# Optimization experiments

Hardware: AMD Instinct MI355X
Metric: run time of the kernel (lower is better)

## Reference

```python
import jax, jax.numpy as jnp
import numpy as np

H = 32          # num_attention_heads
D_NOPE = 128    # qk_nope_head_dim
D_ROPE = 64     # qk_rope_head_dim
D_Q = D_NOPE + D_ROPE  # 192, q_head_dim
D_V = 128       # v_head_dim
R_KV = 512      # kv_lora_rank
EPS = 1e-6


def setup_inputs() -> dict:
    key = jax.random.key(0)
    ks = jax.random.split(key, 5)
    return {
        "hidden_states": jax.random.normal(ks[0], (2, 4096, 4096), jnp.float32),
        "q_a_w": jax.random.normal(ks[1], (1536, 4096), jnp.float32) * 0.02,
        "q_b_w": jax.random.normal(ks[2], (H * D_Q, 1536), jnp.float32) * 0.02,
        "kv_a_w": jax.random.normal(ks[3], (R_KV + D_ROPE, 4096), jnp.float32) * 0.02,
        "kv_b_w": jax.random.normal(ks[4], (H * (D_NOPE + D_V), R_KV), jnp.float32) * 0.02,
        "q_a_ln_w": jnp.ones((1536,), jnp.float32),
        "kv_a_ln_w": jnp.ones((R_KV,), jnp.float32),
    }


def _rmsnorm(x, w):
    xf = x.astype(jnp.float32)
    var = jnp.mean(xf * xf, axis=-1, keepdims=True)
    return (w * (xf * jax.lax.rsqrt(var + EPS))).astype(x.dtype)


def _deepseek_transpose(x):
    # interleave swap on last dim: view (..., d//2, 2) -> transpose -> (..., d)
    b, h, s, d = x.shape
    return x.reshape(b, h, s, d // 2, 2).swapaxes(-1, -2).reshape(b, h, s, d)


def reference(hidden_states, q_a_w, q_b_w, kv_a_w, kv_b_w, q_a_ln_w, kv_a_ln_w):
    b, s, _ = hidden_states.shape
    # Q path: low-rank A -> RMSNorm -> B
    q = _rmsnorm(hidden_states @ q_a_w.T, q_a_ln_w) @ q_b_w.T
    q = q.reshape(b, s, H, D_Q).transpose(0, 2, 1, 3)  # [b, H, s, 192]
    q_nope, q_pe = q[..., :D_NOPE], q[..., D_NOPE:]
    # KV path: joint A proj, split compressed_kv / k_pe
    ckv = hidden_states @ kv_a_w.T                      # [b, s, 576]
    compressed_kv, k_pe = ckv[..., :R_KV], ckv[..., R_KV:]
    k_pe = k_pe.reshape(b, s, 1, D_ROPE).transpose(0, 2, 1, 3)  # [b, 1, s, 64]
    kv = _rmsnorm(compressed_kv, kv_a_ln_w) @ kv_b_w.T
    kv = kv.reshape(b, s, H, D_NOPE + D_V).transpose(0, 2, 1, 3)  # [b, H, s, 256]
    k_nope, value_states = kv[..., :D_NOPE], kv[..., D_NOPE:]
    # interleaved rope transpose
    q_pe = _deepseek_transpose(q_pe)
    k_pe = _deepseek_transpose(k_pe)
    query_states = jnp.concatenate([q_nope, q_pe], axis=-1)                     # [b, H, s, 192]
    key_states = jnp.concatenate(
        [k_nope, jnp.broadcast_to(k_pe, (b, H, s, D_ROPE))], axis=-1)           # [b, H, s, 192]
    v_padded = jnp.pad(value_states, ((0, 0), (0, 0), (0, 0), (0, D_Q - D_V)))  # [b, H, s, 192]
    return jnp.concatenate([query_states, key_states, v_padded], axis=1)        # [b, 3H, s, 192]
```

## Files before the change

### kernel.cpp

```cpp
#include <hip/hip_runtime.h>
#include <hip/hip_bf16.h>

typedef __hip_bfloat16 bf16;
typedef __attribute__((ext_vector_type(8))) short short8;
typedef __attribute__((ext_vector_type(4))) float floatx4;

struct bf16x4 { bf16 a, b, c, d; };

#define OUT_BSTRIDE 75497472u
#define OUT_HSTRIDE 786432u

__device__ __forceinline__ void gload_lds16(const bf16* g, bf16* l) {
    __builtin_amdgcn_global_load_lds((const __attribute__((address_space(1))) void*)g,
                                     (__attribute__((address_space(3))) void*)l,
                                     16, 0, 0);
}

__global__ __launch_bounds__(256) void cvt_f32_bf16(const float* __restrict__ src,
                                                    bf16* __restrict__ dst, int n4) {
    const int stride = gridDim.x * blockDim.x;
    for (int i = blockIdx.x * blockDim.x + threadIdx.x; i < n4; i += stride) {
        const float4 v = ((const float4*)src)[i];
        bf16x4 o;
        o.a = __float2bfloat16(v.x);
        o.b = __float2bfloat16(v.y);
        o.c = __float2bfloat16(v.z);
        o.d = __float2bfloat16(v.w);
        ((bf16x4*)dst)[i] = o;
    }
}

template <int MODE>
__global__ __launch_bounds__(256) void gemm_bt(const bf16* __restrict__ A,
                                               const bf16* __restrict__ Bq,
                                               const bf16* __restrict__ Bkv,
                                               bf16* __restrict__ Cq,
                                               bf16* __restrict__ Ckv,
                                               float* __restrict__ Of) {
    constexpr int K   = 4096;
    constexpr int LDA = 4096;
    constexpr int LDB = 4096;

    __shared__ __align__(16) bf16 sA[128 * 32];
    __shared__ __align__(16) bf16 sB[128 * 32];

    const int tid = threadIdx.x;
    const int m0  = blockIdx.x * 128;

    const bf16* Bsel;
    bf16* Cbf = nullptr;
    int n0, nmax = 0x40000000, ldc = 0;
    if (blockIdx.y < 12) {
        Bsel = Bq;  n0 = blockIdx.y * 128;        nmax = 1536; ldc = 1536; Cbf = Cq;
    } else {
        Bsel = Bkv; n0 = (blockIdx.y - 12) * 128; nmax = 576;  ldc = 576;  Cbf = Ckv;
    }

    const int r0 = tid >> 2;
    const int kc = tid & 3;
    const bf16* ga0 = A + (size_t)(m0 + r0) * LDA + kc * 8;
    const bf16* ga1 = ga0 + (size_t)64 * LDA;
    int br0 = n0 + r0;      if (br0 > nmax - 1) br0 = nmax - 1;
    int br1 = n0 + r0 + 64; if (br1 > nmax - 1) br1 = nmax - 1;
    const bf16* gb0 = Bsel + (size_t)br0 * LDB + kc * 8;
    const bf16* gb1 = Bsel + (size_t)br1 * LDB + kc * 8;
    bf16* lA0 = sA + tid * 8;
    bf16* lA1 = sA + (tid + 256) * 8;
    bf16* lB0 = sB + tid * 8;
    bf16* lB1 = sB + (tid + 256) * 8;

    const int lane = tid & 63;
    const int wid  = tid >> 6;
    const int wm   = wid >> 1;
    const int wn   = wid & 1;
    const int ln   = lane & 15;
    const int qo   = (lane >> 4) * 8;

    const short8* pa[4];
    const short8* pb[4];
#pragma unroll
    for (int i = 0; i < 4; ++i) {
        pa[i] = (const short8*)(sA + (wm * 64 + i * 16 + ln) * 32 + qo);
        pb[i] = (const short8*)(sB + (wn * 64 + i * 16 + ln) * 32 + qo);
    }

    floatx4 acc[4][4];
#pragma unroll
    for (int i = 0; i < 4; ++i)
#pragma unroll
        for (int j = 0; j < 4; ++j) acc[i][j] = (floatx4){0.f, 0.f, 0.f, 0.f};

    for (int k0 = 0; k0 < K; k0 += 32) {
        gload_lds16(ga0, lA0);
        gload_lds16(ga1, lA1);
        gload_lds16(gb0, lB0);
        gload_lds16(gb1, lB1);
        ga0 += 32; ga1 += 32; gb0 += 32; gb1 += 32;
        __syncthreads();

        short8 af[4], bfr[4];
#pragma unroll
        for (int i = 0; i < 4; ++i) af[i] = *pa[i];
#pragma unroll
        for (int j = 0; j < 4; ++j) bfr[j] = *pb[j];
#pragma unroll
        for (int i = 0; i < 4; ++i)
#pragma unroll
            for (int j = 0; j < 4; ++j)
                acc[i][j] = __builtin_amdgcn_mfma_f32_16x16x32_bf16(af[i], bfr[j], acc[i][j], 0, 0, 0);
        __syncthreads();
    }

    const int rowq = (lane >> 4) * 4;
#pragma unroll
    for (int j = 0; j < 4; ++j) {
        const int c0 = n0 + wn * 64 + j * 16;
        const int c  = c0 + ln;
        const bool ok = (c < nmax);
#pragma unroll
        for (int i = 0; i < 4; ++i) {
            const int t = m0 + wm * 64 + i * 16 + rowq;
#pragma unroll
            for (int r = 0; r < 4; ++r) {
                if (ok) Cbf[(size_t)(t + r) * ldc + c] = __float2bfloat16(acc[i][j][r]);
            }
        }
    }
}

template <int MODE>
__global__ __launch_bounds__(512) void gemm8(const bf16* __restrict__ A,
                                             const bf16* __restrict__ B,
                                             float* __restrict__ Of) {
    constexpr int K   = (MODE == 1) ? 1536 : 512;
    constexpr int LDA = (MODE == 1) ? 1536 : 576;
    constexpr int LDB = (MODE == 1) ? 1536 : 512;
    constexpr int NT  = K / 64;

    __shared__ __align__(16) bf16 sA[2][2][128 * 64];
    __shared__ __align__(16) bf16 sB[2][2][128 * 64];

    const int tid = threadIdx.x;
    const int m0  = blockIdx.x * 256;
    const int n0  = blockIdx.y * 256;

    const int srow   = tid >> 3;
    const int schunk = (tid & 7) ^ (srow & 7);
    const bf16* gA0 = A + (size_t)(m0 + srow) * LDA + schunk * 8;
    const bf16* gA1 = gA0 + (size_t)64 * LDA;
    const bf16* gB0 = B + (size_t)(n0 + srow) * LDB + schunk * 8;
    const bf16* gB1 = gB0 + (size_t)64 * LDB;

    auto stageA = [&](int bb, int h, int k0) {
        bf16* d = &sA[bb][h][tid * 8];
        const size_t ho = (size_t)h * (128 * LDA) + k0;
        gload_lds16(gA0 + ho, d);
        gload_lds16(gA1 + ho, d + 4096);
    };
    auto stageB = [&](int bb, int h, int k0) {
        bf16* d = &sB[bb][h][tid * 8];
        const size_t ho = (size_t)h * (128 * LDB) + k0;
        gload_lds16(gB0 + ho, d);
        gload_lds16(gB1 + ho, d + 4096);
    };

    const int lane = tid & 63;
    const int wid  = tid >> 6;
    const int wm   = wid >> 2;
    const int wn   = wid & 3;
    const int ln   = lane & 15;
    const int q4   = lane >> 4;
    const int swz  = ln & 7;
    const int aoff0 = ln * 64 + ((q4 ^ swz) * 8);
    const int aoff1 = ln * 64 + (((4 + q4) ^ swz) * 8);

    floatx4 acc[8][4];
#pragma unroll
    for (int i = 0; i < 8; ++i)
#pragma unroll
        for (int j = 0; j < 4; ++j) acc[i][j] = (floatx4){0.f, 0.f, 0.f, 0.f};

    stageA(0, 0, 0);  stageA(0, 1, 0);
    stageB(0, 0, 0);  stageB(0, 1, 0);
    stageA(1, 0, 64); stageA(1, 1, 64);
    asm volatile("s_waitcnt vmcnt(4)" ::: "memory");
    __builtin_amdgcn_s_barrier();
    asm volatile("" ::: "memory");

    short8 a0[4][2], a1[4][2], b0[2][2], b1[2][2];

    for (int c = 0; c < NT; ++c) {
        const int bb = c & 1;
        const bf16* hA = &sA[bb][wm][0];
        const bf16* hB = &sB[bb][wn >> 1][(wn & 1) * 4096];
        const int kn1 = (c + 1) * 64;
        const int kn2 = (c + 2) * 64;

#pragma unroll
        for (int i = 0; i < 4; ++i) {
            a0[i][0] = *(const short8*)(hA + i * 1024 + aoff0);
            a0[i][1] = *(const short8*)(hA + i * 1024 + aoff1);
        }
#pragma unroll
        for (int j = 0; j < 2; ++j) {
            b0[j][0] = *(const short8*)(hB + j * 1024 + aoff0);
            b0[j][1] = *(const short8*)(hB + j * 1024 + aoff1);
        }
        if (c + 1 < NT) stageB(bb ^ 1, 0, kn1);
        __builtin_amdgcn_s_barrier();
        asm volatile("s_waitcnt lgkmcnt(0)" ::: "memory");
        __builtin_amdgcn_s_setprio(1);
#pragma unroll
        for (int i = 0; i < 4; ++i)
#pragma unroll
            for (int j = 0; j < 2; ++j) {
                acc[i][j] = __builtin_amdgcn_mfma_f32_16x16x32_bf16(a0[i][0], b0[j][0], acc[i][j], 0, 0, 0);
                acc[i][j] = __builtin_amdgcn_mfma_f32_16x16x32_bf16(a0[i][1], b0[j][1], acc[i][j], 0, 0, 0);
            }
        __builtin_amdgcn_s_setprio(0);
        __builtin_amdgcn_s_barrier();
        asm volatile("" ::: "memory");

#pragma unroll
        for (int i = 0; i < 4; ++i) {
            a1[i][0] = *(const short8*)(hA + 4096 + i * 1024 + aoff0);
            a1[i][1] = *(const short8*)(hA + 4096 + i * 1024 + aoff1);
        }
        if (c + 1 < NT) stageB(bb ^ 1, 1, kn1);
        __builtin_amdgcn_s_barrier();
        asm volatile("s_waitcnt lgkmcnt(0)" ::: "memory");
        __builtin_amdgcn_s_setprio(1);
#pragma unroll
        for (int i = 0; i < 4; ++i)
#pragma unroll
            for (int j = 0; j < 2; ++j) {
                acc[4 + i][j] = __builtin_amdgcn_mfma_f32_16x16x32_bf16(a1[i][0], b0[j][0], acc[4 + i][j], 0, 0, 0);
                acc[4 + i][j] = __builtin_amdgcn_mfma_f32_16x16x32_bf16(a1[i][1], b0[j][1], acc[4 + i][j], 0, 0, 0);
            }
        __builtin_amdgcn_s_setprio(0);
        __builtin_amdgcn_s_barrier();
        asm volatile("" ::: "memory");

#pragma unroll
        for (int j = 0; j < 2; ++j) {
            b1[j][0] = *(const short8*)(hB + (2 + j) * 1024 + aoff0);
            b1[j][1] = *(const short8*)(hB + (2 + j) * 1024 + aoff1);
        }
        if (c + 2 < NT) stageA(bb, 0, kn2);
        __builtin_amdgcn_s_barrier();
        asm volatile("s_waitcnt lgkmcnt(0)" ::: "memory");
        __builtin_amdgcn_s_setprio(1);
#pragma unroll
        for (int i = 0; i < 4; ++i)
#pragma unroll
            for (int j = 0; j < 2; ++j) {
                acc[i][2 + j] = __builtin_amdgcn_mfma_f32_16x16x32_bf16(a0[i][0], b1[j][0], acc[i][2 + j], 0, 0, 0);
                acc[i][2 + j] = __builtin_amdgcn_mfma_f32_16x16x32_bf16(a0[i][1], b1[j][1], acc[i][2 + j], 0, 0, 0);
            }
        __builtin_amdgcn_s_setprio(0);
        __builtin_amdgcn_s_barrier();
        asm volatile("" ::: "memory");

        if (c + 2 < NT) stageA(bb, 1, kn2);
        __builtin_amdgcn_s_barrier();
        asm volatile("s_waitcnt lgkmcnt(0)" ::: "memory");
        __builtin_amdgcn_s_setprio(1);
#pragma unroll
        for (int i = 0; i < 4; ++i)
#pragma unroll
            for (int j = 0; j < 2; ++j) {
                acc[4 + i][2 + j] = __builtin_amdgcn_mfma_f32_16x16x32_bf16(a1[i][0], b1[j][0], acc[4 + i][2 + j], 0, 0, 0);
                acc[4 + i][2 + j] = __builtin_amdgcn_mfma_f32_16x16x32_bf16(a1[i][1], b1[j][1], acc[4 + i][2 + j], 0, 0, 0);
            }
        __builtin_amdgcn_s_setprio(0);
        if (c + 2 < NT) {
            asm volatile("s_waitcnt vmcnt(4)" ::: "memory");
        } else if (c + 1 < NT) {
            asm volatile("s_waitcnt vmcnt(0)" ::: "memory");
        }
        __builtin_amdgcn_s_barrier();
        asm volatile("" ::: "memory");
    }

#pragma unroll
    for (int nj = 0; nj < 4; ++nj) {
        const int c0 = n0 + wn * 64 + nj * 16;
        size_t colbase;
        if constexpr (MODE == 1) {
            const int h  = c0 / 192;
            const int e0 = c0 - h * 192;
            const int e  = e0 + ln;
            int d;
            if (e0 >= 128) {
                const int p = e - 128;
                d = 128 + (p & 1) * 32 + (p >> 1);
            } else {
                d = e;
            }
            colbase = (size_t)h * OUT_HSTRIDE + d;
        } else {
            const int h  = c0 >> 8;
            const int e0 = c0 & 255;
            const int e  = e0 + ln;
            const int head = (e0 < 128) ? (32 + h) : (64 + h);
            const int d    = (e0 < 128) ? e : (e - 128);
            colbase = (size_t)head * OUT_HSTRIDE + d;
        }
#pragma unroll
        for (int mi = 0; mi < 8; ++mi) {
            const int tbase = m0 + wm * 128 + mi * 16 + q4 * 4;
#pragma unroll
            for (int r = 0; r < 4; ++r) {
                const int t  = tbase + r;
                const int b2 = t >> 12;
                const int ss = t & 4095;
                Of[(size_t)b2 * OUT_BSTRIDE + (size_t)ss * 192 + colbase] = acc[mi][nj][r];
            }
        }
    }
}

__global__ __launch_bounds__(256) void norm_kpe(bf16* __restrict__ q_a,
                                                bf16* __restrict__ ckv,
                                                const float* __restrict__ qw,
                                                const float* __restrict__ kw,
                                                float* __restrict__ out) {
    __shared__ float red[4];
    __shared__ float skpe[64];
    const int tid = threadIdx.x;
    const int r   = blockIdx.x;

    if (r < 8192) {
        bf16* row = q_a + (size_t)r * 1536;
        float x[6];
#pragma unroll
        for (int k = 0; k < 6; ++k) x[k] = __bfloat162float(row[tid + k * 256]);
        float ss = 0.f;
#pragma unroll
        for (int k = 0; k < 6; ++k) ss += x[k] * x[k];
#pragma unroll
        for (int o = 32; o > 0; o >>= 1) ss += __shfl_down(ss, o, 64);
        if ((tid & 63) == 0) red[tid >> 6] = ss;
        __syncthreads();
        const float tot   = red[0] + red[1] + red[2] + red[3];
        const float scale = rsqrtf(tot * (1.0f / 1536.0f) + 1e-6f);
#pragma unroll
        for (int k = 0; k < 6; ++k) {
            const float w = qw[tid + k * 256];
            row[tid + k * 256] = __float2bfloat16(x[k] * scale * w);
        }
    } else {
        const int t = r - 8192;
        bf16* row   = ckv + (size_t)t * 576;
        float x0 = __bfloat162float(row[tid]);
        float x1 = __bfloat162float(row[tid + 256]);
        if (tid < 64) skpe[tid] = __bfloat162float(row[512 + tid]);
        float ss = x0 * x0 + x1 * x1;
#pragma unroll
        for (int o = 32; o > 0; o >>= 1) ss += __shfl_down(ss, o, 64);
        if ((tid & 63) == 0) red[tid >> 6] = ss;
        __syncthreads();
        const float tot   = red[0] + red[1] + red[2] + red[3];
        const float scale = rsqrtf(tot * (1.0f / 512.0f) + 1e-6f);
        row[tid]       = __float2bfloat16(x0 * scale * kw[tid]);
        row[tid + 256] = __float2bfloat16(x1 * scale * kw[tid + 256]);

        const int i  = tid & 63;
        const int hg = tid >> 6;
        const float v = skpe[2 * (i & 31) + (i >> 5)];
        const int bb  = t >> 12;
        const int ssx = t & 4095;
        float* obase = out + (size_t)bb * OUT_BSTRIDE + (size_t)ssx * 192 + 128 + i;
#pragma unroll
        for (int h = 0; h < 8; ++h) {
            const int head = hg * 8 + h;
            obase[(size_t)(32 + head) * OUT_HSTRIDE] = v;
            obase[(size_t)(64 + head) * OUT_HSTRIDE] = 0.0f;
        }
    }
}

extern "C" void kernel_launch(void* const* d_in, const int* in_sizes, int n_in,
                              void* d_out, int out_size, void* d_ws, size_t ws_size,
                              hipStream_t stream) {
    const float* hidden = (const float*)d_in[0];
    const float* q_a_w  = (const float*)d_in[1];
    const float* q_b_w  = (const float*)d_in[2];
    const float* kv_a_w = (const float*)d_in[3];
    const float* kv_b_w = (const float*)d_in[4];
    const float* q_ln   = (const float*)d_in[5];
    const float* kv_ln  = (const float*)d_in[6];
    float* out = (float*)d_out;

    bf16* hid_b  = (bf16*)d_ws;
    bf16* qaw_b  = hid_b + (size_t)8192 * 4096;
    bf16* qbw_b  = qaw_b + (size_t)1536 * 4096;
    bf16* kvaw_b = qbw_b + (size_t)6144 * 1536;
    bf16* kvbw_b = kvaw_b + (size_t)576 * 4096;
    bf16* q_a    = kvbw_b + (size_t)8192 * 512;
    bf16* ckv    = q_a + (size_t)8192 * 1536;

    dim3 blk(256);
    dim3 blk8(512);
    cvt_f32_bf16<<<dim3(4096), blk, 0, stream>>>(hidden, hid_b, 8192 * 4096 / 4);
    cvt_f32_bf16<<<dim3(1024), blk, 0, stream>>>(q_a_w, qaw_b, 1536 * 4096 / 4);
    cvt_f32_bf16<<<dim3(1024), blk, 0, stream>>>(q_b_w, qbw_b, 6144 * 1536 / 4);
    cvt_f32_bf16<<<dim3(512),  blk, 0, stream>>>(kv_a_w, kvaw_b, 576 * 4096 / 4);
    cvt_f32_bf16<<<dim3(512),  blk, 0, stream>>>(kv_b_w, kvbw_b, 8192 * 512 / 4);

    gemm_bt<0><<<dim3(64, 17), blk, 0, stream>>>(hid_b, qaw_b, kvaw_b, q_a, ckv, nullptr);
    norm_kpe<<<dim3(16384), blk, 0, stream>>>(q_a, ckv, q_ln, kv_ln, out);
    gemm8<1><<<dim3(32, 24), blk8, 0, stream>>>(q_a, qbw_b, out);
    gemm8<2><<<dim3(32, 32), blk8, 0, stream>>>(ckv, kvbw_b, out);
}
```

Before: 1.234 ms.

## Route the A-projection GEMM through the pipelined 256x256 gemm8 kernel with block swizzle

Drops the simple single-buffered 128x128 gemm_bt kernel for the fused q_a/kv_a projection and runs it through a new MODE 0 of the double-buffered, LDS-swizzled 256x256 gemm8 kernel, with clamped B rows and bf16 output. It also adds a linear-to-swizzled block index remap across all gemm8 launches so that neighbouring workgroups share tiles in cache. The larger tiles should raise reuse and hide load latency on the K=4096 GEMM. In exchange, the kv part (576 columns in three 256-wide tiles) wastes compute on padding, and the 32x9 grid gives fewer workgroups.

New measurement: 1.305 ms. 1.06x slower.

```diff
diff --git a/kernel.cpp b/kernel.cpp
--- a/kernel.cpp
+++ b/kernel.cpp
@@ -31,137 +31,62 @@
 }
 
 template <int MODE>
-__global__ __launch_bounds__(256) void gemm_bt(const bf16* __restrict__ A,
-                                               const bf16* __restrict__ Bq,
-                                               const bf16* __restrict__ Bkv,
-                                               bf16* __restrict__ Cq,
-                                               bf16* __restrict__ Ckv,
-                                               float* __restrict__ Of) {
-    constexpr int K   = 4096;
-    constexpr int LDA = 4096;
-    constexpr int LDB = 4096;
-
-    __shared__ __align__(16) bf16 sA[128 * 32];
-    __shared__ __align__(16) bf16 sB[128 * 32];
-
-    const int tid = threadIdx.x;
-    const int m0  = blockIdx.x * 128;
-
-    const bf16* Bsel;
-    bf16* Cbf = nullptr;
-    int n0, nmax = 0x40000000, ldc = 0;
-    if (blockIdx.y < 12) {
-        Bsel = Bq;  n0 = blockIdx.y * 128;        nmax = 1536; ldc = 1536; Cbf = Cq;
-    } else {
-        Bsel = Bkv; n0 = (blockIdx.y - 12) * 128; nmax = 576;  ldc = 576;  Cbf = Ckv;
-    }
-
-    const int r0 = tid >> 2;
-    const int kc = tid & 3;
-    const bf16* ga0 = A + (size_t)(m0 + r0) * LDA + kc * 8;
-    const bf16* ga1 = ga0 + (size_t)64 * LDA;
-    int br0 = n0 + r0;      if (br0 > nmax - 1) br0 = nmax - 1;
-    int br1 = n0 + r0 + 64; if (br1 > nmax - 1) br1 = nmax - 1;
-    const bf16* gb0 = Bsel + (size_t)br0 * LDB + kc * 8;
-    const bf16* gb1 = Bsel + (size_t)br1 * LDB + kc * 8;
-    bf16* lA0 = sA + tid * 8;
-    bf16* lA1 = sA + (tid + 256) * 8;
-    bf16* lB0 = sB + tid * 8;
-    bf16* lB1 = sB + (tid + 256) * 8;
-
-    const int lane = tid & 63;
-    const int wid  = tid >> 6;
-    const int wm   = wid >> 1;
-    const int wn   = wid & 1;
-    const int ln   = lane & 15;
-    const int qo   = (lane >> 4) * 8;
-
-    const short8* pa[4];
-    const short8* pb[4];
-#pragma unroll
-    for (int i = 0; i < 4; ++i) {
-        pa[i] = (const short8*)(sA + (wm * 64 + i * 16 + ln) * 32 + qo);
-        pb[i] = (const short8*)(sB + (wn * 64 + i * 16 + ln) * 32 + qo);
-    }
-
-    floatx4 acc[4][4];
-#pragma unroll
-    for (int i = 0; i < 4; ++i)
-#pragma unroll
-        for (int j = 0; j < 4; ++j) acc[i][j] = (floatx4){0.f, 0.f, 0.f, 0.f};
-
-    for (int k0 = 0; k0 < K; k0 += 32) {
-        gload_lds16(ga0, lA0);
-        gload_lds16(ga1, lA1);
-        gload_lds16(gb0, lB0);
-        gload_lds16(gb1, lB1);
-        ga0 += 32; ga1 += 32; gb0 += 32; gb1 += 32;
-        __syncthreads();
-
-        short8 af[4], bfr[4];
-#pragma unroll
-        for (int i = 0; i < 4; ++i) af[i] = *pa[i];
-#pragma unroll
-        for (int j = 0; j < 4; ++j) bfr[j] = *pb[j];
-#pragma unroll
-        for (int i = 0; i < 4; ++i)
-#pragma unroll
-            for (int j = 0; j < 4; ++j)
-                acc[i][j] = __builtin_amdgcn_mfma_f32_16x16x32_bf16(af[i], bfr[j], acc[i][j], 0, 0, 0);
-        __syncthreads();
-    }
-
-    const int rowq = (lane >> 4) * 4;
-#pragma unroll
-    for (int j = 0; j < 4; ++j) {
-        const int c0 = n0 + wn * 64 + j * 16;
-        const int c  = c0 + ln;
-        const bool ok = (c < nmax);
-#pragma unroll
-        for (int i = 0; i < 4; ++i) {
-            const int t = m0 + wm * 64 + i * 16 + rowq;
-#pragma unroll
-            for (int r = 0; r < 4; ++r) {
-                if (ok) Cbf[(size_t)(t + r) * ldc + c] = __float2bfloat16(acc[i][j][r]);
-            }
-        }
-    }
-}
-
-template <int MODE>
 __global__ __launch_bounds__(512) void gemm8(const bf16* __restrict__ A,
-                                             const bf16* __restrict__ B,
+                                             const bf16* __restrict__ Bq,
+                                             const bf16* __restrict__ Bkv,
+                                             bf16* __restrict__ Cq,
+                                             bf16* __restrict__ Ckv,
                                              float* __restrict__ Of) {
-    constexpr int K   = (MODE == 1) ? 1536 : 512;
-    constexpr int LDA = (MODE == 1) ? 1536 : 576;
-    constexpr int LDB = (MODE == 1) ? 1536 : 512;
+    constexpr int K   = (MODE == 0) ? 4096 : (MODE == 1) ? 1536 : 512;
+    constexpr int LDA = (MODE == 0) ? 4096 : (MODE == 1) ? 1536 : 576;
+    constexpr int LDB = (MODE == 0) ? 4096 : (MODE == 1) ? 1536 : 512;
     constexpr int NT  = K / 64;
 
     __shared__ __align__(16) bf16 sA[2][2][128 * 64];
     __shared__ __align__(16) bf16 sB[2][2][128 * 64];
 
     const int tid = threadIdx.x;
-    const int m0  = blockIdx.x * 256;
-    const int n0  = blockIdx.y * 256;
+
+    const int nwg = 32 * gridDim.y;
+    const int lin = blockIdx.y * 32 + blockIdx.x;
+    const int cpx = nwg >> 3;
+    const int swb = (lin & 7) * cpx + (lin >> 3);
+    const int bx  = swb & 31;
+    const int by  = swb >> 5;
+
+    const int m0 = bx * 256;
+
+    const bf16* Bsel;
+    bf16* Cb = nullptr;
+    int n0, nmax = 0x40000000, ldc = 0;
+    if constexpr (MODE == 0) {
+        if (by < 6) { Bsel = Bq;  n0 = by * 256;       nmax = 1536; ldc = 1536; Cb = Cq; }
+        else        { Bsel = Bkv; n0 = (by - 6) * 256; nmax = 576;  ldc = 576;  Cb = Ckv; }
+    } else {
+        Bsel = Bq; n0 = by * 256;
+    }
 
     const int srow   = tid >> 3;
     const int schunk = (tid & 7) ^ (srow & 7);
-    const bf16* gA0 = A + (size_t)(m0 + srow) * LDA + schunk * 8;
-    const bf16* gA1 = gA0 + (size_t)64 * LDA;
-    const bf16* gB0 = B + (size_t)(n0 + srow) * LDB + schunk * 8;
-    const bf16* gB1 = gB0 + (size_t)64 * LDB;
+    const bf16* gA[4];
+    const bf16* gB[4];
+#pragma unroll
+    for (int g = 0; g < 4; ++g) {
+        gA[g] = A + (size_t)(m0 + srow + g * 64) * LDA + schunk * 8;
+        int rr = n0 + srow + g * 64;
+        if constexpr (MODE == 0) { if (rr > nmax - 1) rr = nmax - 1; }
+        gB[g] = Bsel + (size_t)rr * LDB + schunk * 8;
+    }
 
     auto stageA = [&](int bb, int h, int k0) {
         bf16* d = &sA[bb][h][tid * 8];
-        const size_t ho = (size_t)h * (128 * LDA) + k0;
-        gload_lds16(gA0 + ho, d);
-        gload_lds16(gA1 + ho, d + 4096);
+        gload_lds16(gA[2 * h] + k0, d);
+        gload_lds16(gA[2 * h + 1] + k0, d + 4096);
     };
     auto stageB = [&](int bb, int h, int k0) {
         bf16* d = &sB[bb][h][tid * 8];
-        const size_t ho = (size_t)h * (128 * LDB) + k0;
-        gload_lds16(gB0 + ho, d);
-        gload_lds16(gB1 + ho, d + 4096);
+        gload_lds16(gB[2 * h] + k0, d);
+        gload_lds16(gB[2 * h + 1] + k0, d + 4096);
     };
 
     const int lane = tid & 63;
@@ -285,36 +210,50 @@
 #pragma unroll
     for (int nj = 0; nj < 4; ++nj) {
         const int c0 = n0 + wn * 64 + nj * 16;
-        size_t colbase;
-        if constexpr (MODE == 1) {
-            const int h  = c0 / 192;
-            const int e0 = c0 - h * 192;
-            const int e  = e0 + ln;
-            int d;
-            if (e0 >= 128) {
-                const int p = e - 128;
-                d = 128 + (p & 1) * 32 + (p >> 1);
+        const int c  = c0 + ln;
+
+        if constexpr (MODE == 0) {
+            const bool ok = (c < nmax);
+#pragma unroll
+            for (int mi = 0; mi < 8; ++mi) {
+                const int tb = m0 + wm * 128 + mi * 16 + q4 * 4;
+#pragma unroll
+                for (int r = 0; r < 4; ++r) {
+                    if (ok) Cb[(size_t)(tb + r) * ldc + c] = __float2bfloat16(acc[mi][nj][r]);
+                }
+            }
+        } else {
+            size_t colbase;
+            if constexpr (MODE == 1) {
+                const int h  = c0 / 192;
+                const int e0 = c0 - h * 192;
+                const int e  = e0 + ln;
+                int d;
+                if (e0 >= 128) {
+                    const int p = e - 128;
+                    d = 128 + (p & 1) * 32 + (p >> 1);
+                } else {
+                    d = e;
+                }
+                colbase = (size_t)h * OUT_HSTRIDE + d;
             } else {
-                d = e;
-            }
-            colbase = (size_t)h * OUT_HSTRIDE + d;
-        } else {
-            const int h  = c0 >> 8;
-            const int e0 = c0 & 255;
-            const int e  = e0 + ln;
-            const int head = (e0 < 128) ? (32 + h) : (64 + h);
-            const int d    = (e0 < 128) ? e : (e - 128);
-            colbase = (size_t)head * OUT_HSTRIDE + d;
-        }
-#pragma unroll
-        for (int mi = 0; mi < 8; ++mi) {
-            const int tbase = m0 + wm * 128 + mi * 16 + q4 * 4;
-#pragma unroll
-            for (int r = 0; r < 4; ++r) {
-                const int t  = tbase + r;
-                const int b2 = t >> 12;
-                const int ss = t & 4095;
-                Of[(size_t)b2 * OUT_BSTRIDE + (size_t)ss * 192 + colbase] = acc[mi][nj][r];
+                const int h  = c0 >> 8;
+                const int e0 = c0 & 255;
+                const int e  = e0 + ln;
+                const int head = (e0 < 128) ? (32 + h) : (64 + h);
+                const int d    = (e0 < 128) ? e : (e - 128);
+                colbase = (size_t)head * OUT_HSTRIDE + d;
+            }
+#pragma unroll
+            for (int mi = 0; mi < 8; ++mi) {
+                const int tbase = m0 + wm * 128 + mi * 16 + q4 * 4;
+#pragma unroll
+                for (int r = 0; r < 4; ++r) {
+                    const int t  = tbase + r;
+                    const int b2 = t >> 12;
+                    const int ss = t & 4095;
+                    Of[(size_t)b2 * OUT_BSTRIDE + (size_t)ss * 192 + colbase] = acc[mi][nj][r];
+                }
             }
         }
     }
@@ -408,8 +347,8 @@
     cvt_f32_bf16<<<dim3(512),  blk, 0, stream>>>(kv_a_w, kvaw_b, 576 * 4096 / 4);
     cvt_f32_bf16<<<dim3(512),  blk, 0, stream>>>(kv_b_w, kvbw_b, 8192 * 512 / 4);
 
-    gemm_bt<0><<<dim3(64, 17), blk, 0, stream>>>(hid_b, qaw_b, kvaw_b, q_a, ckv, nullptr);
+    gemm8<0><<<dim3(32, 9),  blk8, 0, stream>>>(hid_b, qaw_b, kvaw_b, q_a, ckv, nullptr);
     norm_kpe<<<dim3(16384), blk, 0, stream>>>(q_a, ckv, q_ln, kv_ln, out);
-    gemm8<1><<<dim3(32, 24), blk8, 0, stream>>>(q_a, qbw_b, out);
-    gemm8<2><<<dim3(32, 32), blk8, 0, stream>>>(ckv, kvbw_b, out);
-}
+    gemm8<1><<<dim3(32, 24), blk8, 0, stream>>>(q_a, qbw_b, nullptr, nullptr, nullptr, out);
+    gemm8<2><<<dim3(32, 32), blk8, 0, stream>>>(ckv, kvbw_b, nullptr, nullptr, nullptr, out);
+}
```
